# Kernel optimization log

Measured on AMD Instinct MI355X. Metric: run time of the kernel, lower is better.

Reference implementation:

```python
import jax, jax.numpy as jnp
import numpy as np

NF, VOCAB, E, ST, L, BATCH = 39, 10000, 128, 16, 4, 2048
SEQ = NF + 1  # cls token + fields


def setup_inputs() -> dict:
    key = jax.random.key(0)
    ks = jax.random.split(key, 16)
    se = 1.0 / np.sqrt(E)
    s2e = 1.0 / np.sqrt(2 * E)
    inp = {
        "x": jax.random.randint(ks[0], (BATCH, NF), 0, VOCAB),
        "emb_table": jax.random.normal(ks[1], (NF, VOCAB + 1, E), jnp.float32) * 0.02,
        "cls_token": jax.random.normal(ks[2], (1, 1, E), jnp.float32) * 0.02,
        "ln_g": jnp.ones((L, 2, E), jnp.float32),
        "ln_b": jnp.zeros((L, 2, E), jnp.float32),
        "xproj_w": jax.random.normal(ks[3], (L, 2, E, 2 * E), jnp.float32) * se,
        "xproj_b": jnp.zeros((L, 2, 2 * E), jnp.float32),
        "A": jax.random.uniform(ks[4], (L, 2, E, ST), jnp.float32, -0.01, 0.01),
        "D": jnp.ones((L, 2, E), jnp.float32),
        "outproj_w": jax.random.normal(ks[5], (L, 2, E, E), jnp.float32) * se,
        "outproj_b": jnp.zeros((L, 2, E), jnp.float32),
        "merge_w": jax.random.normal(ks[6], (L, 2 * E, E), jnp.float32) * s2e,
        "merge_b": jnp.zeros((L, E), jnp.float32),
        "w1": jax.random.normal(ks[7], (E, 128), jnp.float32) * se,
        "b1": jnp.zeros((128,), jnp.float32),
        "w2": jax.random.normal(ks[8], (128, 64), jnp.float32) * (1.0 / np.sqrt(128)),
        "b2": jnp.zeros((64,), jnp.float32),
        "w3": jax.random.normal(ks[9], (64, 1), jnp.float32) * 0.125,
        "b3": jnp.zeros((1,), jnp.float32),
    }
    return inp


def _layernorm(x, g, b, eps=1e-5):
    m = x.mean(-1, keepdims=True)
    v = ((x - m) ** 2).mean(-1, keepdims=True)
    return (x - m) * jax.lax.rsqrt(v + eps) * g + b


def _mamba_block(x, g, bb, wx, bx, A, D, wo, bo):
    # x: [b, s, e]
    res = x
    xn = _layernorm(x, g, bb)
    xp = xn @ wx + bx                       # [b, s, 2e]
    delta, Bm = jnp.split(xp, 2, axis=-1)
    delta = jax.nn.softplus(delta)
    # torch: h = cumsum(xn*B)[...,None]; out = (h * exp(delta[...,None]*A)).sum(-1)
    # equivalent: out = cumsum(xn*B) * exp(delta[...,None]*A).sum(-1)
    s = jnp.exp(delta[..., None] * A).sum(-1)   # [b, s, e] (4D intermediate [b,s,e,st])
    h = jnp.cumsum(xn * Bm, axis=1)             # [b, s, e]
    out = h * s + xn * D
    return out @ wo + bo + res


def _forward(x, emb_table, cls_token, ln_g, ln_b, xproj_w, xproj_b, A, D,
             outproj_w, outproj_b, merge_w, merge_b, w1, b1, w2, b2, w3, b3):
    batch = x.shape[0]
    emb = emb_table.at[:, 0, :].set(0.0)        # padding_idx=0 rows zeroed
    seq = emb[jnp.arange(NF)[None, :], x]       # [b, nf, e]
    cls = jnp.broadcast_to(cls_token, (batch, 1, E))
    seq = jnp.concatenate([cls, seq], axis=1)   # [b, nf+1, e]

    def body(carry, p):
        g, bb, wx, bx, Ap, Dp, wo, bo, mw, mb = p
        f = _mamba_block(carry, g[0], bb[0], wx[0], bx[0], Ap[0], Dp[0], wo[0], bo[0])
        bk = _mamba_block(carry[:, ::-1], g[1], bb[1], wx[1], bx[1],
                          Ap[1], Dp[1], wo[1], bo[1])[:, ::-1]
        out = jnp.concatenate([f, bk], axis=-1) @ mw + mb
        return out, None

    seq, _ = jax.lax.scan(body, seq, (ln_g, ln_b, xproj_w, xproj_b, A, D,
                                      outproj_w, outproj_b, merge_w, merge_b))
    h = seq[:, 0, :]
    h = jax.nn.relu(h @ w1 + b1)
    h = jax.nn.relu(h @ w2 + b2)
    return (h @ w3 + b3)[:, 0]                  # [batch] logits


def reference(x, emb_table, cls_token, ln_g, ln_b, xproj_w, xproj_b, A, D,
              outproj_w, outproj_b, merge_w, merge_b, w1, b1, w2, b2, w3, b3):
    return _forward(x, emb_table, cls_token, ln_g, ln_b, xproj_w, xproj_b, A, D,
                    outproj_w, outproj_b, merge_w, merge_b, w1, b1, w2, b2, w3, b3)
```

## Files before the change

### kernel.cpp

```cpp
#include <hip/hip_runtime.h>

#define NFEAT   39
#define SEQL    40
#define EDIM    128
#define NSTATE  16
#define NLAYERS 4
#define VROWS   10001

typedef __attribute__((ext_vector_type(8))) short short8;
typedef __attribute__((ext_vector_type(4))) float f32x4;

__device__ __forceinline__ float b2f(unsigned short u) {
  unsigned v = ((unsigned)u) << 16;
  return __builtin_bit_cast(float, v);
}
__device__ __forceinline__ unsigned short f2b(float f) {
  unsigned u = __builtin_bit_cast(unsigned, f);
  u += 0x7FFFu + ((u >> 16) & 1u);
  return (unsigned short)(u >> 16);
}
__device__ __forceinline__ float ldin(const void* p, long i, int bf) {
  if (bf) return b2f(((const unsigned short*)p)[i]);
  return ((const float*)p)[i];
}

#define OFF_CLS 0
#define OFF_LNG 128
#define OFF_LNB 1152
#define OFF_XB  2176
#define OFF_AC  4224
#define OFF_D   8320
#define OFF_OB  9344
#define OFF_MB  10368
#define OFF_W1  10880
#define OFF_B1  27264
#define OFF_W2  27392
#define OFF_B2  35584
#define OFF_W3  35648
#define OFF_B3  35712
#define NF32    35713

#define NPK_XW  262144
#define NPK_WO  131072
#define NPK_MW  131072

struct SrcPtrs { const void* p[19]; };

__global__ void convert_kernel(SrcPtrs sp, float* W, unsigned short* pkxw,
                               unsigned short* pkwo, unsigned short* pkmw,
                               int* flag) {
  unsigned w0 = *(const unsigned*)sp.p[3];
  int bf = (w0 != 0x3F800000u) ? 1 : 0;
  if (blockIdx.x == 0 && threadIdx.x == 0) *flag = bf;
  const int T0 = NF32;
  const int T1 = T0 + NPK_XW;
  const int T2 = T1 + NPK_WO;
  const int T3 = T2 + NPK_MW;
  for (int i = blockIdx.x * blockDim.x + threadIdx.x; i < T3;
       i += gridDim.x * blockDim.x) {
    if (i < T0) {
      if (i >= OFF_AC && i < OFF_D) {
        int o  = i - OFF_AC;
        int c  = o & 3;
        int e  = (o >> 2) & 127;
        int pd = o >> 9;
        const void* s = sp.p[7];
        float acc = 0.f;
        for (int k = 0; k < 16; ++k) {
          float a = bf ? b2f(((const unsigned short*)s)[(pd * 128 + e) * 16 + k])
                       : ((const float*)s)[(pd * 128 + e) * 16 + k];
          float p = a;
          if (c >= 1) p *= a;
          if (c >= 2) p *= a;
          if (c >= 3) p *= a;
          acc += p;
        }
        const float inv = (c == 0) ? 1.f : (c == 1) ? 0.5f
                        : (c == 2) ? (1.f / 6.f) : (1.f / 24.f);
        W[i] = acc * inv;
      } else {
        const void* s; int li;
        if      (i < OFF_LNG) { s = sp.p[2];  li = i - OFF_CLS; }
        else if (i < OFF_LNB) { s = sp.p[3];  li = i - OFF_LNG; }
        else if (i < OFF_XB)  { s = sp.p[4];  li = i - OFF_LNB; }
        else if (i < OFF_AC)  { s = sp.p[6];  li = i - OFF_XB; }
        else if (i < OFF_OB)  { s = sp.p[8];  li = i - OFF_D; }
        else if (i < OFF_MB)  { s = sp.p[10]; li = i - OFF_OB; }
        else if (i < OFF_W1)  { s = sp.p[12]; li = i - OFF_MB; }
        else if (i < OFF_B1)  { s = sp.p[13]; li = i - OFF_W1; }
        else if (i < OFF_W2)  { s = sp.p[14]; li = i - OFF_B1; }
        else if (i < OFF_B2)  { s = sp.p[15]; li = i - OFF_W2; }
        else if (i < OFF_W3)  { s = sp.p[16]; li = i - OFF_B2; }
        else if (i < OFF_B3)  { s = sp.p[17]; li = i - OFF_W3; }
        else                  { s = sp.p[18]; li = i - OFF_B3; }
        W[i] = bf ? b2f(((const unsigned short*)s)[li]) : ((const float*)s)[li];
      }
    } else if (i < T1) {
      int o = i - T0;
      int j = o & 7, lane = (o >> 3) & 63, kb = (o >> 9) & 3;
      int nt = (o >> 11) & 15, pd = o >> 15;
      int k = kb * 32 + (lane >> 4) * 8 + j;
      int n = nt * 16 + (lane & 15);
      float v = bf ? b2f(((const unsigned short*)sp.p[5])[(pd * 128 + k) * 256 + n])
                   : ((const float*)sp.p[5])[(pd * 128 + k) * 256 + n];
      pkxw[o] = f2b(v);
    } else if (i < T2) {
      int o = i - T1;
      int j = o & 7, lane = (o >> 3) & 63, kb = (o >> 9) & 3;
      int nt = (o >> 11) & 7, pd = o >> 14;
      int k = kb * 32 + (lane >> 4) * 8 + j;
      int n = nt * 16 + (lane & 15);
      float v = bf ? b2f(((const unsigned short*)sp.p[9])[(pd * 128 + k) * 128 + n])
                   : ((const float*)sp.p[9])[(pd * 128 + k) * 128 + n];
      pkwo[o] = f2b(v);
    } else {
      int o = i - T2;
      int j = o & 7, lane = (o >> 3) & 63, kb = (o >> 9) & 7;
      int nt = (o >> 12) & 7, l = o >> 15;
      int k = kb * 32 + (lane >> 4) * 8 + j;
      int n = nt * 16 + (lane & 15);
      float v = bf ? b2f(((const unsigned short*)sp.p[11])[(l * 256 + k) * 128 + n])
                   : ((const float*)sp.p[11])[(l * 256 + k) * 128 + n];
      pkmw[o] = f2b(v);
    }
  }
}

#define SXB_OFF  0
#define SHO_OFF  10880
#define SF_OFF   21760
#define SCAR_OFF 32640
#define LDS_TOT  53760

__global__ __launch_bounds__(256, 3)
void mamba_kernel(const int* __restrict__ x, const void* __restrict__ emb,
                  const float* __restrict__ W,
                  const unsigned short* __restrict__ pkxw,
                  const unsigned short* __restrict__ pkwo,
                  const unsigned short* __restrict__ pkmw,
                  const int* __restrict__ flagp, void* __restrict__ outp) {
  __shared__ __align__(16) unsigned char sMem[LDS_TOT];
  unsigned short* sXB  = (unsigned short*)(sMem + SXB_OFF);
  unsigned short* sHO  = (unsigned short*)(sMem + SHO_OFF);
  unsigned short* sF   = (unsigned short*)(sMem + SF_OFF);
  float*          sCar = (float*)        (sMem + SCAR_OFF);

  const int b    = blockIdx.x;
  const int tid  = threadIdx.x;
  const int w    = tid >> 6;
  const int lane = tid & 63;
  const int q    = lane >> 4;
  const int li   = lane & 15;
  const int bf   = *flagp;

  for (int i = tid; i < SEQL * EDIM; i += 256) {
    int t = i >> 7, e = i & 127;
    float v;
    if (t == 0) v = W[OFF_CLS + e];
    else {
      int f = t - 1;
      int idx = x[b * NFEAT + f];
      v = (idx == 0) ? 0.f : ldin(emb, ((long)f * VROWS + idx) * EDIM + e, bf);
    }
    sCar[t * 132 + e] = v;
  }
  __syncthreads();

  for (int l = 0; l < NLAYERS; ++l) {
    for (int dir = 0; dir < 2; ++dir) {
      const int pd = l * 2 + dir;
      const float* g  = W + OFF_LNG + pd * EDIM;
      const float* bb = W + OFF_LNB + pd * EDIM;
      const float* bx = W + OFF_XB + pd * 256;
      const float* AC = W + OFF_AC + pd * 512;
      const float* Dp = W + OFF_D  + pd * EDIM;
      const float* bo = W + OFF_OB + pd * EDIM;

      for (int t = w; t < SEQL; t += 4) {
        float v0 = sCar[t * 132 + lane], v1 = sCar[t * 132 + lane + 64];
        float sum = v0 + v1;
        for (int m = 32; m; m >>= 1) sum += __shfl_xor(sum, m, 64);
        float mean = sum * (1.f / 128.f);
        float d0 = v0 - mean, d1 = v1 - mean;
        float vs = d0 * d0 + d1 * d1;
        for (int m = 32; m; m >>= 1) vs += __shfl_xor(vs, m, 64);
        float inv = rsqrtf(vs * (1.f / 128.f) + 1e-5f);
        sXB[t * 136 + lane]      = f2b(d0 * inv * g[lane]      + bb[lane]);
        sXB[t * 136 + lane + 64] = f2b(d1 * inv * g[lane + 64] + bb[lane + 64]);
      }
      __syncthreads();

      for (int cti = 0; cti < 2; ++cti) {
        const int ct = w + cti * 4;
        const int e  = ct * 16 + li;
        short8 Bd[4], Bb4[4];
#pragma unroll
        for (int kb = 0; kb < 4; ++kb) {
          Bd[kb]  = *(const short8*)(pkxw + (((pd * 16 + ct)     * 4 + kb) * 64 + lane) * 8);
          Bb4[kb] = *(const short8*)(pkxw + (((pd * 16 + ct + 8) * 4 + kb) * 64 + lane) * 8);
        }
        const float4 cv = *(const float4*)(AC + e * 4);
        float bxd = bx[e], bxb = bx[128 + e], Dv = Dp[e];
        float sv[3][4], xnv[3][4], pv[3][4];
#pragma unroll
        for (int m = 0; m < 3; ++m) {
          f32x4 aD = {0.f, 0.f, 0.f, 0.f}, aB = {0.f, 0.f, 0.f, 0.f};
#pragma unroll
          for (int kb = 0; kb < 4; ++kb) {
            const short8 afr = *(const short8*)(sXB + (m * 16 + li) * 136 + kb * 32 + q * 8);
            aD = __builtin_amdgcn_mfma_f32_16x16x32_bf16(afr, Bd[kb],  aD, 0, 0, 0);
            aB = __builtin_amdgcn_mfma_f32_16x16x32_bf16(afr, Bb4[kb], aB, 0, 0, 0);
          }
#pragma unroll
          for (int r = 0; r < 4; ++r) {
            int t = m * 16 + q * 4 + r;
            float xd  = aD[r] + bxd;
            float spv = fmaxf(xd, 0.f) + __logf(1.f + __expf(-fabsf(xd)));
            float s = 16.f + spv * (cv.x + spv * (cv.y + spv * (cv.z + spv * cv.w)));
            sv[m][r] = s;
            float xn = b2f(sXB[t * 136 + e]);
            xnv[m][r] = xn;
            float p = xn * (aB[r] + bxb);
            pv[m][r] = (t < SEQL) ? p : 0.f;
          }
        }
        if (dir == 0) {
          float base = 0.f;
#pragma unroll
          for (int m = 0; m < 3; ++m) {
            float p0 = pv[m][0], p1 = p0 + pv[m][1];
            float p2 = p1 + pv[m][2], p3 = p2 + pv[m][3];
            float c  = p3;
            float e1 = __shfl_up(c, 16, 64);
            float e2 = __shfl_up(c, 32, 64);
            float e3 = __shfl_up(c, 48, 64);
            float ex = (q >= 1 ? e1 : 0.f) + (q >= 2 ? e2 : 0.f) + (q >= 3 ? e3 : 0.f);
            float tot = __shfl(ex + c, 48 + li, 64);
            pv[m][0] = base + ex + p0; pv[m][1] = base + ex + p1;
            pv[m][2] = base + ex + p2; pv[m][3] = base + ex + p3;
            base += tot;
          }
        } else {
          float base = 0.f;
#pragma unroll
          for (int m = 2; m >= 0; --m) {
            float p3 = pv[m][3], p2 = p3 + pv[m][2];
            float p1 = p2 + pv[m][1], p0 = p1 + pv[m][0];
            float c  = p0;
            float e1 = __shfl_down(c, 16, 64);
            float e2 = __shfl_down(c, 32, 64);
            float e3 = __shfl_down(c, 48, 64);
            float ex = (q <= 2 ? e1 : 0.f) + (q <= 1 ? e2 : 0.f) + (q <= 0 ? e3 : 0.f);
            float tot = __shfl(ex + c, li, 64);
            pv[m][0] = base + ex + p0; pv[m][1] = base + ex + p1;
            pv[m][2] = base + ex + p2; pv[m][3] = base + ex + p3;
            base += tot;
          }
        }
#pragma unroll
        for (int m = 0; m < 3; ++m)
#pragma unroll
          for (int r = 0; r < 4; ++r) {
            int t = m * 16 + q * 4 + r;
            if (t < SEQL)
              sHO[t * 136 + e] = f2b(pv[m][r] * sv[m][r] + xnv[m][r] * Dv);
          }
      }
      __syncthreads();

      {
        unsigned short* dst = dir ? sXB : sF;
        for (int nti = 0; nti < 2; ++nti) {
          const int nt = w + nti * 4;
          const int n  = nt * 16 + li;
          short8 Bf[4];
#pragma unroll
          for (int kb = 0; kb < 4; ++kb)
            Bf[kb] = *(const short8*)(pkwo + (((pd * 8 + nt) * 4 + kb) * 64 + lane) * 8);
          float bov = bo[n];
#pragma unroll
          for (int m = 0; m < 3; ++m) {
            f32x4 ac = {0.f, 0.f, 0.f, 0.f};
#pragma unroll
            for (int kb = 0; kb < 4; ++kb) {
              const short8 afr = *(const short8*)(sHO + (m * 16 + li) * 136 + kb * 32 + q * 8);
              ac = __builtin_amdgcn_mfma_f32_16x16x32_bf16(afr, Bf[kb], ac, 0, 0, 0);
            }
#pragma unroll
            for (int r = 0; r < 4; ++r) {
              int t = m * 16 + q * 4 + r;
              if (t < SEQL)
                dst[t * 136 + n] = f2b(ac[r] + bov + sCar[t * 132 + n]);
            }
          }
        }
      }
      __syncthreads();
    }

    {
      const float* mb = W + OFF_MB + l * EDIM;
      for (int nti = 0; nti < 2; ++nti) {
        const int nt = w + nti * 4;
        const int n  = nt * 16 + li;
        short8 Bf[8];
#pragma unroll
        for (int kb = 0; kb < 8; ++kb)
          Bf[kb] = *(const short8*)(pkmw + (((l * 8 + nt) * 8 + kb) * 64 + lane) * 8);
        float mbv = mb[n];
#pragma unroll
        for (int m = 0; m < 3; ++m) {
          f32x4 ac = {0.f, 0.f, 0.f, 0.f};
#pragma unroll
          for (int kb = 0; kb < 4; ++kb) {
            const short8 afr = *(const short8*)(sF + (m * 16 + li) * 136 + kb * 32 + q * 8);
            ac = __builtin_amdgcn_mfma_f32_16x16x32_bf16(afr, Bf[kb], ac, 0, 0, 0);
          }
#pragma unroll
          for (int kb = 4; kb < 8; ++kb) {
            const short8 afr = *(const short8*)(sXB + (m * 16 + li) * 136 + (kb - 4) * 32 + q * 8);
            ac = __builtin_amdgcn_mfma_f32_16x16x32_bf16(afr, Bf[kb], ac, 0, 0, 0);
          }
#pragma unroll
          for (int r = 0; r < 4; ++r) {
            int t = m * 16 + q * 4 + r;
            if (t < SEQL) sCar[t * 132 + n] = ac[r] + mbv;
          }
        }
      }
    }
    __syncthreads();
  }

  if (tid < 128) {
    float a = W[OFF_B1 + tid];
    const float* w1p = W + OFF_W1;
    for (int e = 0; e < EDIM; e += 4) {
      float4 hv = *(const float4*)&sCar[e];
      a = fmaf(hv.x, w1p[(e + 0) * 128 + tid],
          fmaf(hv.y, w1p[(e + 1) * 128 + tid],
          fmaf(hv.z, w1p[(e + 2) * 128 + tid],
          fmaf(hv.w, w1p[(e + 3) * 128 + tid], a))));
    }
    sCar[132 + tid] = fmaxf(a, 0.f);
  }
  __syncthreads();
  if (tid < 64) {
    float a = W[OFF_B2 + tid];
    const float* w2p = W + OFF_W2;
    for (int i = 0; i < 128; ++i) a = fmaf(sCar[132 + i], w2p[i * 64 + tid], a);
    a = fmaxf(a, 0.f);
    float v = a * W[OFF_W3 + tid];
    for (int m = 32; m; m >>= 1) v += __shfl_xor(v, m, 64);
    if (tid == 0) {
      float res = v + W[OFF_B3];
      if (bf) ((unsigned short*)outp)[b] = f2b(res);
      else    ((float*)outp)[b] = res;
    }
  }
}

extern "C" void kernel_launch(void* const* d_in, const int* in_sizes, int n_in,
                              void* d_out, int out_size, void* d_ws, size_t ws_size,
                              hipStream_t stream) {
  (void)in_sizes; (void)n_in; (void)out_size; (void)ws_size;

  SrcPtrs sp;
  for (int k = 0; k < 19; ++k) sp.p[k] = d_in[k];

  int*            flag = (int*)d_ws;
  float*          Wf   = (float*)((char*)d_ws + 256);
  unsigned short* pkxw = (unsigned short*)((char*)d_ws + 256 + 200704);
  unsigned short* pkwo = pkxw + NPK_XW;
  unsigned short* pkmw = pkwo + NPK_WO;

  convert_kernel<<<dim3(512), dim3(256), 0, stream>>>(sp, Wf, pkxw, pkwo, pkmw, flag);
  mamba_kernel<<<dim3(2048), dim3(256), 0, stream>>>(
      (const int*)d_in[0], d_in[1], Wf, pkxw, pkwo, pkmw, flag, d_out);
}
```

Measured before the change: 621.6 us.

## Fold out-projection and residual into merge weights, hoist layernorm per layer

Precomputes Wo·Mw for each direction, the summed merge weights for the residual path, and the combined biases, all in the convert kernel. This removes the per-direction out-projection GEMM and its barrier from the main kernel. The LN gamma and beta are folded into the x-projection weights and bias, so layernorm now runs once per layer instead of once per direction. In exchange the convert kernel does 128-length dot products per packed element, and products rounded to bf16 may slightly change numerics.

```diff
diff --git a/kernel.cpp b/kernel.cpp
--- a/kernel.cpp
+++ b/kernel.cpp
@@ -41,22 +41,22 @@
 #define NF32    35713
 
 #define NPK_XW  262144
-#define NPK_WO  131072
-#define NPK_MW  131072
+#define NPK_V   65536
 
 struct SrcPtrs { const void* p[19]; };
 
 __global__ void convert_kernel(SrcPtrs sp, float* W, unsigned short* pkxw,
-                               unsigned short* pkwo, unsigned short* pkmw,
-                               int* flag) {
+                               unsigned short* pkv0, unsigned short* pkv1,
+                               unsigned short* pkmr, int* flag) {
   unsigned w0 = *(const unsigned*)sp.p[3];
   int bf = (w0 != 0x3F800000u) ? 1 : 0;
   if (blockIdx.x == 0 && threadIdx.x == 0) *flag = bf;
   const int T0 = NF32;
   const int T1 = T0 + NPK_XW;
-  const int T2 = T1 + NPK_WO;
-  const int T3 = T2 + NPK_MW;
-  for (int i = blockIdx.x * blockDim.x + threadIdx.x; i < T3;
+  const int T2 = T1 + NPK_V;
+  const int T3 = T2 + NPK_V;
+  const int T4 = T3 + NPK_V;
+  for (int i = blockIdx.x * blockDim.x + threadIdx.x; i < T4;
        i += gridDim.x * blockDim.x) {
     if (i < T0) {
       if (i >= OFF_AC && i < OFF_D) {
@@ -64,11 +64,9 @@
         int c  = o & 3;
         int e  = (o >> 2) & 127;
         int pd = o >> 9;
-        const void* s = sp.p[7];
         float acc = 0.f;
         for (int k = 0; k < 16; ++k) {
-          float a = bf ? b2f(((const unsigned short*)s)[(pd * 128 + e) * 16 + k])
-                       : ((const float*)s)[(pd * 128 + e) * 16 + k];
+          float a = ldin(sp.p[7], (pd * 128 + e) * 16 + k, bf);
           float p = a;
           if (c >= 1) p *= a;
           if (c >= 2) p *= a;
@@ -78,22 +76,42 @@
         const float inv = (c == 0) ? 1.f : (c == 1) ? 0.5f
                         : (c == 2) ? (1.f / 6.f) : (1.f / 24.f);
         W[i] = acc * inv;
+      } else if (i >= OFF_XB && i < OFF_AC) {
+        int o = i - OFF_XB;
+        int pd = o >> 8, n = o & 255;
+        float acc = ldin(sp.p[6], o, bf);
+        for (int k = 0; k < 128; ++k) {
+          float bbk = ldin(sp.p[4], pd * 128 + k, bf);
+          float wxk = ldin(sp.p[5], ((long)(pd * 128 + k)) * 256 + n, bf);
+          acc = fmaf(bbk, wxk, acc);
+        }
+        W[i] = acc;
+      } else if (i >= OFF_MB && i < OFF_W1) {
+        int o = i - OFF_MB;
+        int l = o >> 7, n = o & 127;
+        float acc = ldin(sp.p[12], o, bf);
+        for (int k = 0; k < 128; ++k) {
+          float bo0 = ldin(sp.p[10], (l * 2) * 128 + k, bf);
+          float bo1 = ldin(sp.p[10], (l * 2 + 1) * 128 + k, bf);
+          float mwt = ldin(sp.p[11], ((long)(l * 256 + k)) * 128 + n, bf);
+          float mwb = ldin(sp.p[11], ((long)(l * 256 + 128 + k)) * 128 + n, bf);
+          acc = fmaf(bo0, mwt, fmaf(bo1, mwb, acc));
+        }
+        W[i] = acc;
       } else {
         const void* s; int li;
         if      (i < OFF_LNG) { s = sp.p[2];  li = i - OFF_CLS; }
         else if (i < OFF_LNB) { s = sp.p[3];  li = i - OFF_LNG; }
         else if (i < OFF_XB)  { s = sp.p[4];  li = i - OFF_LNB; }
-        else if (i < OFF_AC)  { s = sp.p[6];  li = i - OFF_XB; }
         else if (i < OFF_OB)  { s = sp.p[8];  li = i - OFF_D; }
         else if (i < OFF_MB)  { s = sp.p[10]; li = i - OFF_OB; }
-        else if (i < OFF_W1)  { s = sp.p[12]; li = i - OFF_MB; }
         else if (i < OFF_B1)  { s = sp.p[13]; li = i - OFF_W1; }
         else if (i < OFF_W2)  { s = sp.p[14]; li = i - OFF_B1; }
         else if (i < OFF_B2)  { s = sp.p[15]; li = i - OFF_W2; }
         else if (i < OFF_W3)  { s = sp.p[16]; li = i - OFF_B2; }
         else if (i < OFF_B3)  { s = sp.p[17]; li = i - OFF_W3; }
         else                  { s = sp.p[18]; li = i - OFF_B3; }
-        W[i] = bf ? b2f(((const unsigned short*)s)[li]) : ((const float*)s)[li];
+        W[i] = ldin(s, li, bf);
       }
     } else if (i < T1) {
       int o = i - T0;
@@ -101,27 +119,31 @@
       int nt = (o >> 11) & 15, pd = o >> 15;
       int k = kb * 32 + (lane >> 4) * 8 + j;
       int n = nt * 16 + (lane & 15);
-      float v = bf ? b2f(((const unsigned short*)sp.p[5])[(pd * 128 + k) * 256 + n])
-                   : ((const float*)sp.p[5])[(pd * 128 + k) * 256 + n];
+      float g = ldin(sp.p[3], pd * 128 + k, bf);
+      float v = ldin(sp.p[5], ((long)(pd * 128 + k)) * 256 + n, bf) * g;
       pkxw[o] = f2b(v);
-    } else if (i < T2) {
-      int o = i - T1;
+    } else {
+      int which = (i < T2) ? 0 : (i < T3) ? 1 : 2;
+      int o = i - (which == 0 ? T1 : which == 1 ? T2 : T3);
       int j = o & 7, lane = (o >> 3) & 63, kb = (o >> 9) & 3;
-      int nt = (o >> 11) & 7, pd = o >> 14;
+      int nt = (o >> 11) & 7, l = o >> 14;
       int k = kb * 32 + (lane >> 4) * 8 + j;
       int n = nt * 16 + (lane & 15);
-      float v = bf ? b2f(((const unsigned short*)sp.p[9])[(pd * 128 + k) * 128 + n])
-                   : ((const float*)sp.p[9])[(pd * 128 + k) * 128 + n];
-      pkwo[o] = f2b(v);
-    } else {
-      int o = i - T2;
-      int j = o & 7, lane = (o >> 3) & 63, kb = (o >> 9) & 7;
-      int nt = (o >> 12) & 7, l = o >> 15;
-      int k = kb * 32 + (lane >> 4) * 8 + j;
-      int n = nt * 16 + (lane & 15);
-      float v = bf ? b2f(((const unsigned short*)sp.p[11])[(l * 256 + k) * 128 + n])
-                   : ((const float*)sp.p[11])[(l * 256 + k) * 128 + n];
-      pkmw[o] = f2b(v);
+      float acc = 0.f;
+      if (which == 2) {
+        acc = ldin(sp.p[11], ((long)(l * 256 + k)) * 128 + n, bf)
+            + ldin(sp.p[11], ((long)(l * 256 + 128 + k)) * 128 + n, bf);
+        pkmr[o] = f2b(acc);
+      } else {
+        int pd = l * 2 + which;
+        int mrow0 = l * 256 + which * 128;
+        for (int m = 0; m < 128; ++m) {
+          float wo = ldin(sp.p[9], ((long)(pd * 128 + k)) * 128 + m, bf);
+          float mw = ldin(sp.p[11], ((long)(mrow0 + m)) * 128 + n, bf);
+          acc = fmaf(wo, mw, acc);
+        }
+        if (which == 0) pkv0[o] = f2b(acc); else pkv1[o] = f2b(acc);
+      }
     }
   }
 }
@@ -136,8 +158,9 @@
 void mamba_kernel(const int* __restrict__ x, const void* __restrict__ emb,
                   const float* __restrict__ W,
                   const unsigned short* __restrict__ pkxw,
-                  const unsigned short* __restrict__ pkwo,
-                  const unsigned short* __restrict__ pkmw,
+                  const unsigned short* __restrict__ pkv0,
+                  const unsigned short* __restrict__ pkv1,
+                  const unsigned short* __restrict__ pkmr,
                   const int* __restrict__ flagp, void* __restrict__ outp) {
   __shared__ __align__(16) unsigned char sMem[LDS_TOT];
   unsigned short* sXB  = (unsigned short*)(sMem + SXB_OFF);
@@ -167,28 +190,28 @@
   __syncthreads();
 
   for (int l = 0; l < NLAYERS; ++l) {
+    for (int t = w; t < SEQL; t += 4) {
+      float v0 = sCar[t * 132 + lane], v1 = sCar[t * 132 + lane + 64];
+      float sum = v0 + v1;
+      for (int m = 32; m; m >>= 1) sum += __shfl_xor(sum, m, 64);
+      float mean = sum * (1.f / 128.f);
+      float d0 = v0 - mean, d1 = v1 - mean;
+      float vs = d0 * d0 + d1 * d1;
+      for (int m = 32; m; m >>= 1) vs += __shfl_xor(vs, m, 64);
+      float inv = rsqrtf(vs * (1.f / 128.f) + 1e-5f);
+      sXB[t * 136 + lane]      = f2b(d0 * inv);
+      sXB[t * 136 + lane + 64] = f2b(d1 * inv);
+    }
+    __syncthreads();
+
     for (int dir = 0; dir < 2; ++dir) {
       const int pd = l * 2 + dir;
-      const float* g  = W + OFF_LNG + pd * EDIM;
-      const float* bb = W + OFF_LNB + pd * EDIM;
       const float* bx = W + OFF_XB + pd * 256;
       const float* AC = W + OFF_AC + pd * 512;
+      const float* gP = W + OFF_LNG + pd * EDIM;
+      const float* bP = W + OFF_LNB + pd * EDIM;
       const float* Dp = W + OFF_D  + pd * EDIM;
-      const float* bo = W + OFF_OB + pd * EDIM;
-
-      for (int t = w; t < SEQL; t += 4) {
-        float v0 = sCar[t * 132 + lane], v1 = sCar[t * 132 + lane + 64];
-        float sum = v0 + v1;
-        for (int m = 32; m; m >>= 1) sum += __shfl_xor(sum, m, 64);
-        float mean = sum * (1.f / 128.f);
-        float d0 = v0 - mean, d1 = v1 - mean;
-        float vs = d0 * d0 + d1 * d1;
-        for (int m = 32; m; m >>= 1) vs += __shfl_xor(vs, m, 64);
-        float inv = rsqrtf(vs * (1.f / 128.f) + 1e-5f);
-        sXB[t * 136 + lane]      = f2b(d0 * inv * g[lane]      + bb[lane]);
-        sXB[t * 136 + lane + 64] = f2b(d1 * inv * g[lane + 64] + bb[lane + 64]);
-      }
-      __syncthreads();
+      unsigned short* dst = dir ? sF : sHO;
 
       for (int cti = 0; cti < 2; ++cti) {
         const int ct = w + cti * 4;
@@ -200,7 +223,8 @@
           Bb4[kb] = *(const short8*)(pkxw + (((pd * 16 + ct + 8) * 4 + kb) * 64 + lane) * 8);
         }
         const float4 cv = *(const float4*)(AC + e * 4);
-        float bxd = bx[e], bxb = bx[128 + e], Dv = Dp[e];
+        float bxd = bx[e], bxb = bx[128 + e];
+        float gv = gP[e], bbv = bP[e], Dv = Dp[e];
         float sv[3][4], xnv[3][4], pv[3][4];
 #pragma unroll
         for (int m = 0; m < 3; ++m) {
@@ -218,7 +242,7 @@
             float spv = fmaxf(xd, 0.f) + __logf(1.f + __expf(-fabsf(xd)));
             float s = 16.f + spv * (cv.x + spv * (cv.y + spv * (cv.z + spv * cv.w)));
             sv[m][r] = s;
-            float xn = b2f(sXB[t * 136 + e]);
+            float xn = fmaf(b2f(sXB[t * 136 + e]), gv, bbv);
             xnv[m][r] = xn;
             float p = xn * (aB[r] + bxb);
             pv[m][r] = (t < SEQL) ? p : 0.f;
@@ -263,63 +287,48 @@
           for (int r = 0; r < 4; ++r) {
             int t = m * 16 + q * 4 + r;
             if (t < SEQL)
-              sHO[t * 136 + e] = f2b(pv[m][r] * sv[m][r] + xnv[m][r] * Dv);
+              dst[t * 136 + e] = f2b(pv[m][r] * sv[m][r] + xnv[m][r] * Dv);
           }
       }
       __syncthreads();
-
-      {
-        unsigned short* dst = dir ? sXB : sF;
-        for (int nti = 0; nti < 2; ++nti) {
-          const int nt = w + nti * 4;
-          const int n  = nt * 16 + li;
-          short8 Bf[4];
-#pragma unroll
-          for (int kb = 0; kb < 4; ++kb)
-            Bf[kb] = *(const short8*)(pkwo + (((pd * 8 + nt) * 4 + kb) * 64 + lane) * 8);
-          float bov = bo[n];
-#pragma unroll
-          for (int m = 0; m < 3; ++m) {
-            f32x4 ac = {0.f, 0.f, 0.f, 0.f};
-#pragma unroll
-            for (int kb = 0; kb < 4; ++kb) {
-              const short8 afr = *(const short8*)(sHO + (m * 16 + li) * 136 + kb * 32 + q * 8);
-              ac = __builtin_amdgcn_mfma_f32_16x16x32_bf16(afr, Bf[kb], ac, 0, 0, 0);
-            }
-#pragma unroll
-            for (int r = 0; r < 4; ++r) {
-              int t = m * 16 + q * 4 + r;
-              if (t < SEQL)
-                dst[t * 136 + n] = f2b(ac[r] + bov + sCar[t * 132 + n]);
-            }
-          }
-        }
-      }
-      __syncthreads();
-    }
+    }
+
+    for (int i = tid; i < SEQL * EDIM; i += 256) {
+      int t = i >> 7, e = i & 127;
+      sXB[t * 136 + e] = f2b(sCar[t * 132 + e]);
+    }
+    __syncthreads();
 
     {
       const float* mb = W + OFF_MB + l * EDIM;
       for (int nti = 0; nti < 2; ++nti) {
         const int nt = w + nti * 4;
         const int n  = nt * 16 + li;
-        short8 Bf[8];
-#pragma unroll
-        for (int kb = 0; kb < 8; ++kb)
-          Bf[kb] = *(const short8*)(pkmw + (((l * 8 + nt) * 8 + kb) * 64 + lane) * 8);
+        short8 B0[4], B1[4], B2[4];
+#pragma unroll
+        for (int kb = 0; kb < 4; ++kb) {
+          B0[kb] = *(const short8*)(pkv0 + (((l * 8 + nt) * 4 + kb) * 64 + lane) * 8);
+          B1[kb] = *(const short8*)(pkv1 + (((l * 8 + nt) * 4 + kb) * 64 + lane) * 8);
+          B2[kb] = *(const short8*)(pkmr + (((l * 8 + nt) * 4 + kb) * 64 + lane) * 8);
+        }
         float mbv = mb[n];
 #pragma unroll
         for (int m = 0; m < 3; ++m) {
           f32x4 ac = {0.f, 0.f, 0.f, 0.f};
 #pragma unroll
           for (int kb = 0; kb < 4; ++kb) {
-            const short8 afr = *(const short8*)(sF + (m * 16 + li) * 136 + kb * 32 + q * 8);
-            ac = __builtin_amdgcn_mfma_f32_16x16x32_bf16(afr, Bf[kb], ac, 0, 0, 0);
-          }
-#pragma unroll
-          for (int kb = 4; kb < 8; ++kb) {
-            const short8 afr = *(const short8*)(sXB + (m * 16 + li) * 136 + (kb - 4) * 32 + q * 8);
-            ac = __builtin_amdgcn_mfma_f32_16x16x32_bf16(afr, Bf[kb], ac, 0, 0, 0);
+            const short8 a0 = *(const short8*)(sHO + (m * 16 + li) * 136 + kb * 32 + q * 8);
+            ac = __builtin_amdgcn_mfma_f32_16x16x32_bf16(a0, B0[kb], ac, 0, 0, 0);
+          }
+#pragma unroll
+          for (int kb = 0; kb < 4; ++kb) {
+            const short8 a1 = *(const short8*)(sF + (m * 16 + li) * 136 + kb * 32 + q * 8);
+            ac = __builtin_amdgcn_mfma_f32_16x16x32_bf16(a1, B1[kb], ac, 0, 0, 0);
+          }
+#pragma unroll
+          for (int kb = 0; kb < 4; ++kb) {
+            const short8 a2 = *(const short8*)(sXB + (m * 16 + li) * 136 + kb * 32 + q * 8);
+            ac = __builtin_amdgcn_mfma_f32_16x16x32_bf16(a2, B2[kb], ac, 0, 0, 0);
           }
 #pragma unroll
           for (int r = 0; r < 4; ++r) {
@@ -371,10 +380,11 @@
   int*            flag = (int*)d_ws;
   float*          Wf   = (float*)((char*)d_ws + 256);
   unsigned short* pkxw = (unsigned short*)((char*)d_ws + 256 + 200704);
-  unsigned short* pkwo = pkxw + NPK_XW;
-  unsigned short* pkmw = pkwo + NPK_WO;
-
-  convert_kernel<<<dim3(512), dim3(256), 0, stream>>>(sp, Wf, pkxw, pkwo, pkmw, flag);
+  unsigned short* pkv0 = pkxw + NPK_XW;
+  unsigned short* pkv1 = pkv0 + NPK_V;
+  unsigned short* pkmr = pkv1 + NPK_V;
+
+  convert_kernel<<<dim3(512), dim3(256), 0, stream>>>(sp, Wf, pkxw, pkv0, pkv1, pkmr, flag);
   mamba_kernel<<<dim3(2048), dim3(256), 0, stream>>>(
-      (const int*)d_in[0], d_in[1], Wf, pkxw, pkwo, pkmw, flag, d_out);
-}
+      (const int*)d_in[0], d_in[1], Wf, pkxw, pkv0, pkv1, pkmr, flag, d_out);
+}
```

Measured after the change: 566.1 us. -8.9%, faster.
